# Performance work log

Measured on AMD Instinct MI355X. Metric: run time of the kernel, lower is better.

The kernel has to match this reference:

```python
import jax, jax.numpy as jnp
import numpy as np


def _rbf_forward(batches, centers, beta, W, b):
    # Pairwise Euclidean distances via GEMM expansion instead of materializing
    # the O(n*K*dim) difference tensor the torch code builds.
    x2 = jnp.sum(batches * batches, axis=1, keepdims=True)          # [n, 1]
    c2 = jnp.sum(centers * centers, axis=1)                          # [K]
    xc = jnp.einsum('nd,kd->nk', batches, centers)                   # [n, K]
    d2 = jnp.maximum(x2 + c2[None, :] - 2.0 * xc, 0.0)               # [n, K]
    dist = jnp.sqrt(d2)
    radial = jnp.exp(-beta * dist)                                   # beta: [1, K]
    return radial @ W.T + b                                          # [n, num_class]


def setup_inputs() -> dict:
    key = jax.random.key(0)
    k1, k2, k3, k4, k5 = jax.random.split(key, 5)
    n, K, dim, num_class = 16384, 2048, 512, 10
    batches = jax.random.normal(k1, (n, dim), dtype=jnp.float32)
    centers = jax.random.normal(k2, (K, dim), dtype=jnp.float32)
    beta = jnp.full((1, K), 0.1, dtype=jnp.float32)  # torch init: ones/10
    W = jax.random.normal(k4, (num_class, K), dtype=jnp.float32) / np.sqrt(K)
    b = jax.random.normal(k5, (num_class,), dtype=jnp.float32) * 0.01
    return {"batches": batches, "centers": centers, "beta": beta, "W": W, "b": b}


def reference(batches, centers, beta, W, b):
    return _rbf_forward(batches, centers, beta, W, b)
```

## Files before the change

### kernel.cpp

```cpp
#include <hip/hip_runtime.h>
#include <hip/hip_bf16.h>
#include <stdint.h>

#define M_N  16384
#define K_C  2048
#define DIM  512
#define NCLS 10
#define NBN  16
#define NBM  (M_N / 128)

typedef unsigned short u16;
typedef float  f32x4  __attribute__((ext_vector_type(4)));
typedef __bf16 bf16x8 __attribute__((ext_vector_type(8)));


__device__ __forceinline__ void async_ld16(const void* g, void* l) {
  __builtin_amdgcn_global_load_lds(
      (const __attribute__((address_space(1))) void*)g,
      (__attribute__((address_space(3))) void*)l,
      16, 0, 0);
}

__device__ __forceinline__ u16 f2bf_rne(float f) {
  uint32_t u = __float_as_uint(f);
  u += 0x7FFFu + ((u >> 16) & 1u);
  return (u16)(u >> 16);
}


#define NPREP ((M_N + K_C) / 2)

__global__ __launch_bounds__(256) void prep(
    const float4* __restrict__ batches, const float4* __restrict__ centers,
    const float* __restrict__ W,
    ushort4* __restrict__ Abf, ushort4* __restrict__ Bbf,
    float* __restrict__ x2, float* __restrict__ c2, u16* __restrict__ Wperm) {
  int b = blockIdx.x, t = threadIdx.x;
  if (b < NPREP) {
    int rp = b * 2 + (t >> 7);
    int col = t & 127;
    const float4* src; ushort4* dst; float* sq; int row;
    if (rp < M_N) { src = batches; dst = Abf; sq = x2; row = rp; }
    else          { src = centers; dst = Bbf; sq = c2; row = rp - M_N; }
    float4 v = src[(size_t)row * 128 + col];
    float ss = v.x * v.x + v.y * v.y + v.z * v.z + v.w * v.w;
    ushort4 o;
    o.x = f2bf_rne(v.x); o.y = f2bf_rne(v.y);
    o.z = f2bf_rne(v.z); o.w = f2bf_rne(v.w);
    dst[(size_t)row * 128 + col] = o;
    ss += __shfl_down(ss, 32);
    ss += __shfl_down(ss, 16);
    ss += __shfl_down(ss, 8);
    ss += __shfl_down(ss, 4);
    ss += __shfl_down(ss, 2);
    ss += __shfl_down(ss, 1);
    __shared__ float part[4];
    if ((t & 63) == 0) part[t >> 6] = ss;
    __syncthreads();
    if (t == 0) sq[row] = part[0] + part[1];
    if (t == 128) sq[row] = part[2] + part[3];
  } else {
    int wb = b - NPREP;
#pragma unroll
    for (int i = 0; i < 4; ++i) {
      int p = wb * 1024 + i * 256 + t;
      int cls = p >> 11, k = p & 2047;
      int bn = k >> 7, rem = k & 127;
      int hh = (rem >> 6) & 1, tt = (rem >> 5) & 1;
      int qq = (rem >> 3) & 3, jj = rem & 7;
      int c = bn * 128 + hh * 64 + (tt * 2 + (jj >> 2)) * 16 + qq * 4 + (jj & 3);
      Wperm[p] = (cls < NCLS) ? f2bf_rne(W[cls * K_C + c]) : (u16)0;
    }
  }
}


__global__ __launch_bounds__(256, 4) void rbf_main(
    const u16* __restrict__ A,
    const u16* __restrict__ B,
    const float* __restrict__ x2,
    const float* __restrict__ c2,
    const float* __restrict__ beta,
    const u16* __restrict__ Wperm,
    float* __restrict__ partial) {
  constexpr int BK = 64;
  __shared__ alignas(16) unsigned char smem[32768];
  u16* As = (u16*)smem;
  u16* Bs = (u16*)(smem + 16384);
  f32x4* sumbuf = (f32x4*)smem;

  const int tid  = threadIdx.x;
  const int lane = tid & 63;
  const int wid  = tid >> 6;
  const int bid = blockIdx.x;
  const int g = bid >> 3, r8 = bid & 7;
  const int bm = r8 * 16 + (g & 15);
  const int bn = g >> 4;
  const int row0 = bm * 128, col0 = bn * 128;
  const int wrC = (wid >> 1) * 64;
  const int wcB = (wid & 1) * 64;

  f32x4 acc[4][4] = {};

  const int srow = tid >> 3;
  const int scol = ((tid & 7) ^ (srow & 7)) * 8;
  const u16* aG = A + (size_t)(row0 + srow) * DIM + scol;
  const u16* bG = B + (size_t)(col0 + srow) * DIM + scol;
  u16* aL = As + tid * 8;
  u16* bL = Bs + tid * 8;

  const int frow = lane & 15;
  const int fq   = lane >> 4;
  const int fsw  = frow & 7;

  for (int k0 = 0; k0 < DIM; k0 += BK) {
    __syncthreads();
#pragma unroll
    for (int i = 0; i < 4; ++i) {
      async_ld16(aG + k0 + i * 32 * DIM, aL + i * 2048);
      async_ld16(bG + k0 + i * 32 * DIM, bL + i * 2048);
    }
    __syncthreads();

#pragma unroll
    for (int kh = 0; kh < 2; ++kh) {
      const int slot = ((kh << 2) | fq) ^ fsw;
      bf16x8 cf[4], bfr[4];
#pragma unroll
      for (int mi = 0; mi < 4; ++mi)
        cf[mi] = *(const bf16x8*)(Bs + (wrC + mi * 16 + frow) * BK + slot * 8);
#pragma unroll
      for (int ni = 0; ni < 4; ++ni)
        bfr[ni] = *(const bf16x8*)(As + (wcB + ni * 16 + frow) * BK + slot * 8);
#pragma unroll
      for (int mi = 0; mi < 4; ++mi)
#pragma unroll
        for (int ni = 0; ni < 4; ++ni)
          acc[mi][ni] = __builtin_amdgcn_mfma_f32_16x16x32_bf16(
              cf[mi], bfr[ni], acc[mi][ni], 0, 0, 0);
    }
  }

  const int cls = lane & 15, q = lane >> 4;
  float4 c2q[4], btq[4];
#pragma unroll
  for (int mi = 0; mi < 4; ++mi) {
    int base = col0 + wrC + mi * 16 + q * 4;
    c2q[mi] = *(const float4*)(c2 + base);
    btq[mi] = *(const float4*)(beta + base);
  }
  float x2v[4];
#pragma unroll
  for (int ni = 0; ni < 4; ++ni)
    x2v[ni] = x2[row0 + wcB + ni * 16 + cls];

#pragma unroll
  for (int mi = 0; mi < 4; ++mi)
#pragma unroll
    for (int ni = 0; ni < 4; ++ni)
#pragma unroll
      for (int r = 0; r < 4; ++r) {
        float xc = acc[mi][ni][r];
        float d2 = fmaxf(x2v[ni] + c2q[mi][r] - 2.0f * xc, 0.0f);
        acc[mi][ni][r] = __expf(-btq[mi][r] * sqrtf(d2));
      }

  const int h = wid >> 1;
  bf16x8 wfr[2];
#pragma unroll
  for (int t = 0; t < 2; ++t)
    wfr[t] = *(const bf16x8*)(Wperm + (size_t)cls * K_C + col0 + h * 64 +
                              t * 32 + q * 8);

  f32x4 acc2[4] = {};
#pragma unroll
  for (int ni = 0; ni < 4; ++ni) {
#pragma unroll
    for (int t = 0; t < 2; ++t) {
      union { u16 hh[8]; bf16x8 v; } pk;
#pragma unroll
      for (int r = 0; r < 4; ++r) {
        pk.hh[r]     = f2bf_rne(acc[2 * t][ni][r]);
        pk.hh[4 + r] = f2bf_rne(acc[2 * t + 1][ni][r]);
      }
      acc2[ni] = __builtin_amdgcn_mfma_f32_16x16x32_bf16(
          pk.v, wfr[t], acc2[ni], 0, 0, 0);
    }
  }

  __syncthreads();
  if (wid >= 2) {
#pragma unroll
    for (int ni = 0; ni < 4; ++ni)
      sumbuf[((wid & 1) * 4 + ni) * 64 + lane] = acc2[ni];
  }
  __syncthreads();
  if (wid < 2) {
#pragma unroll
    for (int ni = 0; ni < 4; ++ni) {
      f32x4 o = sumbuf[(wid * 4 + ni) * 64 + lane];
      acc2[ni] += o;
#pragma unroll
      for (int r = 0; r < 4; ++r) {
        int gr = row0 + wid * 64 + ni * 16 + q * 4 + r;
        __builtin_nontemporal_store(
            acc2[ni][r], &partial[((size_t)bn * M_N + gr) * 16 + cls]);
      }
    }
  }
}


__global__ __launch_bounds__(256) void reduce_out(
    const float* __restrict__ partial, const float* __restrict__ b,
    float* __restrict__ out) {
  int t = threadIdx.x;
  int row = blockIdx.x * 64 + (t >> 2);
  int quad = t & 3;
  f32x4 v = {0.f, 0.f, 0.f, 0.f};
#pragma unroll
  for (int bn = 0; bn < NBN; ++bn) {
    f32x4 p = __builtin_nontemporal_load(
        (const f32x4*)(partial + ((size_t)bn * M_N + row) * 16 + quad * 4));
    v += p;
  }
  if (quad == 0) {
    float4 bq = *(const float4*)b;
    float* o = out + (size_t)row * NCLS;
    *(float2*)o       = {v.x + bq.x, v.y + bq.y};
    *(float2*)(o + 2) = {v.z + bq.z, v.w + bq.w};
  } else if (quad == 1) {
    float4 bq = *(const float4*)(b + 4);
    float* o = out + (size_t)row * NCLS + 4;
    *(float2*)o       = {v.x + bq.x, v.y + bq.y};
    *(float2*)(o + 2) = {v.z + bq.z, v.w + bq.w};
  } else if (quad == 2) {
    *(float2*)(out + (size_t)row * NCLS + 8) = {v.x + b[8], v.y + b[9]};
  }
}


extern "C" void kernel_launch(void* const* d_in, const int* in_sizes, int n_in,
                              void* d_out, int out_size, void* d_ws, size_t ws_size,
                              hipStream_t stream) {
  const float* batches = (const float*)d_in[0];
  const float* centers = (const float*)d_in[1];
  const float* beta    = (const float*)d_in[2];
  const float* W       = (const float*)d_in[3];
  const float* bias    = (const float*)d_in[4];
  float* out = (float*)d_out;

  char* ws = (char*)d_ws;
  u16*  Abf = (u16*)ws;
  u16*  Bbf = (u16*)(ws + (size_t)M_N * DIM * 2);
  float* x2 = (float*)(ws + (size_t)(M_N + K_C) * DIM * 2);
  float* c2 = x2 + M_N;
  u16*  Wpm = (u16*)(c2 + K_C);
  float* partial = (float*)((char*)Wpm + 16 * K_C * 2);

  prep<<<dim3(NPREP + 32), dim3(256), 0, stream>>>(
      (const float4*)batches, (const float4*)centers, W,
      (ushort4*)Abf, (ushort4*)Bbf, x2, c2, Wpm);
  rbf_main<<<dim3(NBN * NBM), dim3(256), 0, stream>>>(
      Abf, Bbf, x2, c2, beta, Wpm, partial);
  reduce_out<<<dim3(M_N / 64), dim3(256), 0, stream>>>(partial, bias, out);
}
```

Measured before the change: 139.8 us.

## Use 256x256 tiles with 8 waves and double-buffered async LDS pipeline

Replaces the 128x128 single-buffered GEMM tile with a 256x256 tile computed by 512 threads, using a double-buffered 128KB LDS layout with global_load_lds prefetch two k-steps ahead. The MFMA work is split into four phases separated by barriers and priority bumps so LDS fragment reads and next-tile loads overlap compute. The goal is to cut the sync stalls and per-tile global traffic of the old loop, and to halve the partial-output slabs to 8. The cost is higher register pressure from 32 accumulators, fewer blocks per CU, and fragile hand-scheduled waitcnt ordering.

```diff
diff --git a/kernel.cpp b/kernel.cpp
--- a/kernel.cpp
+++ b/kernel.cpp
@@ -6,8 +6,9 @@
 #define K_C  2048
 #define DIM  512
 #define NCLS 10
-#define NBN  16
-#define NBM  (M_N / 128)
+#define NBN  8
+#define BKK  64
+#define NSTEP (DIM / BKK)
 
 typedef unsigned short u16;
 typedef float  f32x4  __attribute__((ext_vector_type(4)));
@@ -75,136 +76,200 @@
 }
 
 
-__global__ __launch_bounds__(256, 4) void rbf_main(
-    const u16* __restrict__ A,
-    const u16* __restrict__ B,
+#define SB0 __builtin_amdgcn_sched_barrier(0)
+
+#define PH_OPEN_LGKM do { SB0; __builtin_amdgcn_s_barrier(); \
+    asm volatile("s_waitcnt lgkmcnt(0)" ::: "memory"); SB0; } while (0)
+#define PH_OPEN      do { SB0; __builtin_amdgcn_s_barrier(); SB0; } while (0)
+#define PH_CLOSE     do { SB0; __builtin_amdgcn_s_barrier(); SB0; } while (0)
+
+#define MFMA_Q(MB, NB) do { \
+    __builtin_amdgcn_s_setprio(1); \
+    _Pragma("unroll") for (int mm = 0; mm < 4; ++mm) \
+    _Pragma("unroll") for (int nn = 0; nn < 2; ++nn) \
+    _Pragma("unroll") for (int kh = 0; kh < 2; ++kh) \
+      acc[(MB) + mm][(NB) + nn] = __builtin_amdgcn_mfma_f32_16x16x32_bf16( \
+          cfA[mm][kh], bfB[(NB) + nn][kh], acc[(MB) + mm][(NB) + nn], 0, 0, 0); \
+    __builtin_amdgcn_s_setprio(0); \
+  } while (0)
+
+#define STAGE_A(tt) do { \
+    _Pragma("unroll") for (int h = 0; h < 2; ++h) \
+    _Pragma("unroll") for (int j = 0; j < 2; ++j) \
+      async_ld16(cSrc + (size_t)(h * 128 + j * 64) * DIM + (tt) * BKK, \
+                 smA + ((tt) & 1) * 65536 + h * 16384 + j * 8192 + tid * 16); \
+  } while (0)
+#define STAGE_B(tt) do { \
+    _Pragma("unroll") for (int h = 0; h < 2; ++h) \
+    _Pragma("unroll") for (int j = 0; j < 2; ++j) \
+      async_ld16(bSrc + (size_t)(h * 128 + j * 64) * DIM + (tt) * BKK, \
+                 smB + ((tt) & 1) * 65536 + h * 16384 + j * 8192 + tid * 16); \
+  } while (0)
+
+__global__ __launch_bounds__(512, 2) void rbf_main(
+    const u16* __restrict__ bat,
+    const u16* __restrict__ cen,
     const float* __restrict__ x2,
     const float* __restrict__ c2,
     const float* __restrict__ beta,
     const u16* __restrict__ Wperm,
     float* __restrict__ partial) {
-  constexpr int BK = 64;
-  __shared__ alignas(16) unsigned char smem[32768];
-  u16* As = (u16*)smem;
-  u16* Bs = (u16*)(smem + 16384);
-  f32x4* sumbuf = (f32x4*)smem;
+  __shared__ alignas(16) char smem[131072];
 
   const int tid  = threadIdx.x;
   const int lane = tid & 63;
   const int wid  = tid >> 6;
+  const int wr   = wid >> 2;
+  const int wc   = wid & 3;
+
   const int bid = blockIdx.x;
-  const int g = bid >> 3, r8 = bid & 7;
-  const int bm = r8 * 16 + (g & 15);
-  const int bn = g >> 4;
-  const int row0 = bm * 128, col0 = bn * 128;
-  const int wrC = (wid >> 1) * 64;
-  const int wcB = (wid & 1) * 64;
-
-  f32x4 acc[4][4] = {};
+  const int swz = (bid & 7) * 64 + (bid >> 3);
+  const int bm = swz >> 3;
+  const int bn = swz & 7;
+  const int rb0 = bm * 256;
+  const int cb0 = bn * 256;
 
   const int srow = tid >> 3;
-  const int scol = ((tid & 7) ^ (srow & 7)) * 8;
-  const u16* aG = A + (size_t)(row0 + srow) * DIM + scol;
-  const u16* bG = B + (size_t)(col0 + srow) * DIM + scol;
-  u16* aL = As + tid * 8;
-  u16* bL = Bs + tid * 8;
+  const int swzc = (tid & 7) ^ (srow & 7);
+  const u16* cSrc = cen + (size_t)(cb0 + srow) * DIM + swzc * 8;
+  const u16* bSrc = bat + (size_t)(rb0 + srow) * DIM + swzc * 8;
+  char* smA = smem;
+  char* smB = smem + 32768;
 
   const int frow = lane & 15;
   const int fq   = lane >> 4;
   const int fsw  = frow & 7;
-
-  for (int k0 = 0; k0 < DIM; k0 += BK) {
-    __syncthreads();
-#pragma unroll
-    for (int i = 0; i < 4; ++i) {
-      async_ld16(aG + k0 + i * 32 * DIM, aL + i * 2048);
-      async_ld16(bG + k0 + i * 32 * DIM, bL + i * 2048);
-    }
-    __syncthreads();
-
-#pragma unroll
-    for (int kh = 0; kh < 2; ++kh) {
-      const int slot = ((kh << 2) | fq) ^ fsw;
-      bf16x8 cf[4], bfr[4];
-#pragma unroll
-      for (int mi = 0; mi < 4; ++mi)
-        cf[mi] = *(const bf16x8*)(Bs + (wrC + mi * 16 + frow) * BK + slot * 8);
-#pragma unroll
-      for (int ni = 0; ni < 4; ++ni)
-        bfr[ni] = *(const bf16x8*)(As + (wcB + ni * 16 + frow) * BK + slot * 8);
-#pragma unroll
-      for (int mi = 0; mi < 4; ++mi)
-#pragma unroll
-        for (int ni = 0; ni < 4; ++ni)
-          acc[mi][ni] = __builtin_amdgcn_mfma_f32_16x16x32_bf16(
-              cf[mi], bfr[ni], acc[mi][ni], 0, 0, 0);
-    }
-  }
-
-  const int cls = lane & 15, q = lane >> 4;
-  float4 c2q[4], btq[4];
-#pragma unroll
-  for (int mi = 0; mi < 4; ++mi) {
-    int base = col0 + wrC + mi * 16 + q * 4;
-    c2q[mi] = *(const float4*)(c2 + base);
-    btq[mi] = *(const float4*)(beta + base);
+  const int ck0  = ((0 + fq) ^ fsw) * 16;
+  const int ck1  = ((4 + fq) ^ fsw) * 16;
+  const char* aRd = smem + wr * 16384 + frow * 128;
+  const char* bRd = smem + 32768 + (wc >> 1) * 16384 + (wc & 1) * 8192 + frow * 128;
+
+  f32x4 acc[8][4] = {};
+
+  STAGE_B(0); STAGE_A(0); STAGE_B(1); STAGE_A(1);
+  asm volatile("s_waitcnt vmcnt(8)" ::: "memory");
+  __builtin_amdgcn_s_barrier();
+  SB0;
+
+#pragma unroll
+  for (int t = 0; t < NSTEP; ++t) {
+    const char* Ab = aRd + (t & 1) * 65536;
+    const char* Bb = bRd + (t & 1) * 65536;
+    bf16x8 cfA[4][2], bfB[4][2];
+
+#pragma unroll
+    for (int m = 0; m < 4; ++m) {
+      cfA[m][0] = *(const bf16x8*)(Ab + m * 2048 + ck0);
+      cfA[m][1] = *(const bf16x8*)(Ab + m * 2048 + ck1);
+    }
+#pragma unroll
+    for (int n = 0; n < 2; ++n) {
+      bfB[n][0] = *(const bf16x8*)(Bb + n * 2048 + ck0);
+      bfB[n][1] = *(const bf16x8*)(Bb + n * 2048 + ck1);
+    }
+    PH_OPEN_LGKM;
+    MFMA_Q(0, 0);
+    PH_CLOSE;
+
+#pragma unroll
+    for (int n = 2; n < 4; ++n) {
+      bfB[n][0] = *(const bf16x8*)(Bb + n * 2048 + ck0);
+      bfB[n][1] = *(const bf16x8*)(Bb + n * 2048 + ck1);
+    }
+    PH_OPEN_LGKM;
+    MFMA_Q(0, 2);
+    PH_CLOSE;
+
+#pragma unroll
+    for (int m = 0; m < 4; ++m) {
+      cfA[m][0] = *(const bf16x8*)(Ab + 8192 + m * 2048 + ck0);
+      cfA[m][1] = *(const bf16x8*)(Ab + 8192 + m * 2048 + ck1);
+    }
+    if (t < NSTEP - 2) STAGE_B(t + 2);
+    PH_OPEN_LGKM;
+    MFMA_Q(4, 2);
+    PH_CLOSE;
+
+    if (t < NSTEP - 2) STAGE_A(t + 2);
+    PH_OPEN;
+    MFMA_Q(4, 0);
+    SB0;
+    if (t < NSTEP - 2) {
+      asm volatile("s_waitcnt vmcnt(8)" ::: "memory");
+    } else if (t == NSTEP - 2) {
+      asm volatile("s_waitcnt vmcnt(0)" ::: "memory");
+    }
+    __builtin_amdgcn_s_barrier();
+    SB0;
+  }
+
+  const int cls = frow, q = fq;
+  float4 c2q[8], btq[8];
+#pragma unroll
+  for (int m = 0; m < 8; ++m) {
+    int base = cb0 + wr * 128 + m * 16 + q * 4;
+    c2q[m] = *(const float4*)(c2 + base);
+    btq[m] = *(const float4*)(beta + base);
   }
   float x2v[4];
 #pragma unroll
-  for (int ni = 0; ni < 4; ++ni)
-    x2v[ni] = x2[row0 + wcB + ni * 16 + cls];
-
-#pragma unroll
-  for (int mi = 0; mi < 4; ++mi)
-#pragma unroll
-    for (int ni = 0; ni < 4; ++ni)
+  for (int n = 0; n < 4; ++n)
+    x2v[n] = x2[rb0 + wc * 64 + n * 16 + cls];
+
+#pragma unroll
+  for (int m = 0; m < 8; ++m)
+#pragma unroll
+    for (int n = 0; n < 4; ++n)
 #pragma unroll
       for (int r = 0; r < 4; ++r) {
-        float xc = acc[mi][ni][r];
-        float d2 = fmaxf(x2v[ni] + c2q[mi][r] - 2.0f * xc, 0.0f);
-        acc[mi][ni][r] = __expf(-btq[mi][r] * sqrtf(d2));
+        float xc = acc[m][n][r];
+        float d2 = fmaxf(x2v[n] + c2q[m][r] - 2.0f * xc, 0.0f);
+        acc[m][n][r] = __expf(-btq[m][r] * sqrtf(d2));
       }
 
-  const int h = wid >> 1;
-  bf16x8 wfr[2];
-#pragma unroll
-  for (int t = 0; t < 2; ++t)
-    wfr[t] = *(const bf16x8*)(Wperm + (size_t)cls * K_C + col0 + h * 64 +
-                              t * 32 + q * 8);
+  const int cblk = bn * 2 + wr;
+  bf16x8 wfr[2][2];
+#pragma unroll
+  for (int h = 0; h < 2; ++h)
+#pragma unroll
+    for (int tt = 0; tt < 2; ++tt)
+      wfr[h][tt] = *(const bf16x8*)(Wperm + (size_t)cls * K_C + cblk * 128 +
+                                    h * 64 + tt * 32 + q * 8);
 
   f32x4 acc2[4] = {};
 #pragma unroll
-  for (int ni = 0; ni < 4; ++ni) {
-#pragma unroll
-    for (int t = 0; t < 2; ++t) {
-      union { u16 hh[8]; bf16x8 v; } pk;
+  for (int n = 0; n < 4; ++n)
+#pragma unroll
+    for (int h = 0; h < 2; ++h)
+#pragma unroll
+      for (int tt = 0; tt < 2; ++tt) {
+        union { u16 hh[8]; bf16x8 v; } pk;
+#pragma unroll
+        for (int r = 0; r < 4; ++r) {
+          pk.hh[r]     = f2bf_rne(acc[h * 4 + 2 * tt][n][r]);
+          pk.hh[4 + r] = f2bf_rne(acc[h * 4 + 2 * tt + 1][n][r]);
+        }
+        acc2[n] = __builtin_amdgcn_mfma_f32_16x16x32_bf16(
+            pk.v, wfr[h][tt], acc2[n], 0, 0, 0);
+      }
+
+  f32x4* sumbuf = (f32x4*)smem;
+  if (wr == 1) {
+#pragma unroll
+    for (int n = 0; n < 4; ++n)
+      sumbuf[(wc * 4 + n) * 64 + lane] = acc2[n];
+  }
+  __syncthreads();
+  if (wr == 0) {
+#pragma unroll
+    for (int n = 0; n < 4; ++n) {
+      f32x4 o = sumbuf[(wc * 4 + n) * 64 + lane];
+      acc2[n] += o;
 #pragma unroll
       for (int r = 0; r < 4; ++r) {
-        pk.hh[r]     = f2bf_rne(acc[2 * t][ni][r]);
-        pk.hh[4 + r] = f2bf_rne(acc[2 * t + 1][ni][r]);
-      }
-      acc2[ni] = __builtin_amdgcn_mfma_f32_16x16x32_bf16(
-          pk.v, wfr[t], acc2[ni], 0, 0, 0);
-    }
-  }
-
-  __syncthreads();
-  if (wid >= 2) {
-#pragma unroll
-    for (int ni = 0; ni < 4; ++ni)
-      sumbuf[((wid & 1) * 4 + ni) * 64 + lane] = acc2[ni];
-  }
-  __syncthreads();
-  if (wid < 2) {
-#pragma unroll
-    for (int ni = 0; ni < 4; ++ni) {
-      f32x4 o = sumbuf[(wid * 4 + ni) * 64 + lane];
-      acc2[ni] += o;
-#pragma unroll
-      for (int r = 0; r < 4; ++r) {
-        int gr = row0 + wid * 64 + ni * 16 + q * 4 + r;
+        int gr = rb0 + wc * 64 + n * 16 + q * 4 + r;
         __builtin_nontemporal_store(
-            acc2[ni][r], &partial[((size_t)bn * M_N + gr) * 16 + cls]);
+            acc2[n][r], &partial[((size_t)bn * M_N + gr) * 16 + cls]);
       }
     }
   }
@@ -261,7 +326,7 @@
   prep<<<dim3(NPREP + 32), dim3(256), 0, stream>>>(
       (const float4*)batches, (const float4*)centers, W,
       (ushort4*)Abf, (ushort4*)Bbf, x2, c2, Wpm);
-  rbf_main<<<dim3(NBN * NBM), dim3(256), 0, stream>>>(
+  rbf_main<<<dim3(512), dim3(512), 0, stream>>>(
       Abf, Bbf, x2, c2, beta, Wpm, partial);
   reduce_out<<<dim3(M_N / 64), dim3(256), 0, stream>>>(partial, bias, out);
 }
```

New measurement: 140.0 us. Within noise of the previous version (+0.2%).

## Double-buffer LDS staging with async prefetch two stages ahead in GEMM loop

Applied to the files above, without the earlier changes.

Replaces the single-buffered BK=64 load/sync/compute loop with a double-buffered BK=32 pipeline. Global-to-LDS async loads are issued two stages ahead, tracked with explicit vmcnt waits, and separated by sched barriers and raised wave priority around the MFMA block. The goal is to hide global load latency behind matrix math and remove the full load-then-compute stall each iteration. In exchange there are more iterations, more barriers per K, and a new swizzle layout for the 32-wide tiles, with a risk of subtle waitcnt mistakes.

```diff
diff --git a/kernel.cpp b/kernel.cpp
--- a/kernel.cpp
+++ b/kernel.cpp
@@ -12,6 +12,8 @@
 typedef unsigned short u16;
 typedef float  f32x4  __attribute__((ext_vector_type(4)));
 typedef __bf16 bf16x8 __attribute__((ext_vector_type(8)));
+
+#define SB0 __builtin_amdgcn_sched_barrier(0)
 
 
 __device__ __forceinline__ void async_ld16(const void* g, void* l) {
@@ -83,10 +85,9 @@
     const float* __restrict__ beta,
     const u16* __restrict__ Wperm,
     float* __restrict__ partial) {
-  constexpr int BK = 64;
+  constexpr int BK = 32;
+  constexpr int NST = DIM / BK;
   __shared__ alignas(16) unsigned char smem[32768];
-  u16* As = (u16*)smem;
-  u16* Bs = (u16*)(smem + 16384);
   f32x4* sumbuf = (f32x4*)smem;
 
   const int tid  = threadIdx.x;
@@ -102,52 +103,72 @@
 
   f32x4 acc[4][4] = {};
 
-  const int srow = tid >> 3;
-  const int scol = ((tid & 7) ^ (srow & 7)) * 8;
-  const u16* aG = A + (size_t)(row0 + srow) * DIM + scol;
-  const u16* bG = B + (size_t)(col0 + srow) * DIM + scol;
-  u16* aL = As + tid * 8;
-  u16* bL = Bs + tid * 8;
+  const int srow = tid >> 2;
+  const int sgch = (tid & 3) ^ (srow & 3);
+  const u16* aG = A + (size_t)(row0 + srow) * DIM + sgch * 8;
+  const u16* bG = B + (size_t)(col0 + srow) * DIM + sgch * 8;
+
+#define STAGE(tt) do { \
+    _Pragma("unroll") for (int j = 0; j < 2; ++j) { \
+      async_ld16(bG + (size_t)j * 64 * DIM + (tt) * BK, \
+                 smem + ((tt) & 1) * 16384 + j * 4096 + tid * 16); \
+      async_ld16(aG + (size_t)j * 64 * DIM + (tt) * BK, \
+                 smem + ((tt) & 1) * 16384 + 8192 + j * 4096 + tid * 16); \
+    } \
+  } while (0)
 
   const int frow = lane & 15;
   const int fq   = lane >> 4;
-  const int fsw  = frow & 7;
-
-  for (int k0 = 0; k0 < DIM; k0 += BK) {
-    __syncthreads();
-#pragma unroll
-    for (int i = 0; i < 4; ++i) {
-      async_ld16(aG + k0 + i * 32 * DIM, aL + i * 2048);
-      async_ld16(bG + k0 + i * 32 * DIM, bL + i * 2048);
-    }
-    __syncthreads();
-
-#pragma unroll
-    for (int kh = 0; kh < 2; ++kh) {
-      const int slot = ((kh << 2) | fq) ^ fsw;
-      bf16x8 cf[4], bfr[4];
-#pragma unroll
-      for (int mi = 0; mi < 4; ++mi)
-        cf[mi] = *(const bf16x8*)(Bs + (wrC + mi * 16 + frow) * BK + slot * 8);
+  const int slotB = ((fq ^ (frow & 3)) * 16);
+
+  STAGE(0); STAGE(1);
+  asm volatile("s_waitcnt vmcnt(4)" ::: "memory");
+  __builtin_amdgcn_s_barrier();
+  SB0;
+
+#pragma unroll
+  for (int t = 0; t < NST; ++t) {
+    const unsigned char* base = smem + (t & 1) * 16384;
+    bf16x8 cf[4], bfr[4];
+#pragma unroll
+    for (int mi = 0; mi < 4; ++mi)
+      cf[mi] = *(const bf16x8*)(base + (wrC + mi * 16 + frow) * 64 + slotB);
+#pragma unroll
+    for (int ni = 0; ni < 4; ++ni)
+      bfr[ni] = *(const bf16x8*)(base + 8192 + (wcB + ni * 16 + frow) * 64 + slotB);
+    asm volatile("s_waitcnt lgkmcnt(0)" ::: "memory");
+    SB0;
+    __builtin_amdgcn_s_barrier();
+    SB0;
+
+    if (t < NST - 2) STAGE(t + 2);
+
+    __builtin_amdgcn_s_setprio(1);
+#pragma unroll
+    for (int mi = 0; mi < 4; ++mi)
 #pragma unroll
       for (int ni = 0; ni < 4; ++ni)
-        bfr[ni] = *(const bf16x8*)(As + (wcB + ni * 16 + frow) * BK + slot * 8);
-#pragma unroll
-      for (int mi = 0; mi < 4; ++mi)
-#pragma unroll
-        for (int ni = 0; ni < 4; ++ni)
-          acc[mi][ni] = __builtin_amdgcn_mfma_f32_16x16x32_bf16(
-              cf[mi], bfr[ni], acc[mi][ni], 0, 0, 0);
-    }
+        acc[mi][ni] = __builtin_amdgcn_mfma_f32_16x16x32_bf16(
+            cf[mi], bfr[ni], acc[mi][ni], 0, 0, 0);
+    __builtin_amdgcn_s_setprio(0);
+    SB0;
+
+    if (t < NST - 2) {
+      asm volatile("s_waitcnt vmcnt(4)" ::: "memory");
+    } else if (t == NST - 2) {
+      asm volatile("s_waitcnt vmcnt(0)" ::: "memory");
+    }
+    __builtin_amdgcn_s_barrier();
+    SB0;
   }
 
   const int cls = lane & 15, q = lane >> 4;
   float4 c2q[4], btq[4];
 #pragma unroll
   for (int mi = 0; mi < 4; ++mi) {
-    int base = col0 + wrC + mi * 16 + q * 4;
-    c2q[mi] = *(const float4*)(c2 + base);
-    btq[mi] = *(const float4*)(beta + base);
+    int base2 = col0 + wrC + mi * 16 + q * 4;
+    c2q[mi] = *(const float4*)(c2 + base2);
+    btq[mi] = *(const float4*)(beta + base2);
   }
   float x2v[4];
 #pragma unroll
@@ -208,6 +229,7 @@
       }
     }
   }
+#undef STAGE
 }
 
 
```

After: 140.6 us. No clear change (+0.6%).
